# Kernel tuning notes

Measured on AMD Instinct MI355X. Metric: run time of the kernel, lower is better.

The kernel has to match this reference:

```python
import jax, jax.numpy as jnp
import numpy as np

N = 50000      # nodes
E = 800000     # edges (avg degree 16)
D = 128        # in_dim == hidden_dim
CD = 3         # coord_dim (SE(3))
L = 3          # num_layers


def setup_inputs() -> dict:
    key = jax.random.key(0)
    ks = jax.random.split(key, 10)
    s = np.float32(1.0 / np.sqrt(D))
    return {
        "x": jax.random.normal(ks[0], (N, D), jnp.float32),
        "pos": jax.random.normal(ks[1], (N, CD), jnp.float32),
        "edge_index": jax.random.randint(ks[2], (2, E), 0, N, dtype=jnp.int32),
        # per-layer stacked params (in_dim == hidden_dim so all layers stack)
        "Wl": jax.random.normal(ks[3], (L, D, D), jnp.float32) * s,
        "bl": jnp.zeros((L, D), jnp.float32),
        "Wc": jax.random.normal(ks[4], (L, D, 1), jnp.float32) * s,
        "bc": jnp.zeros((L, 1), jnp.float32),
        "WR": jax.random.normal(ks[5], (L, D, CD * CD), jnp.float32) * s,
        "bR": jnp.zeros((L, CD * CD), jnp.float32),
        "Wt": jax.random.normal(ks[6], (L, D, CD), jnp.float32) * s,
        "bt": jnp.zeros((L, CD), jnp.float32),
        # final fc
        "Wf": jax.random.normal(ks[7], (D, D), jnp.float32) * s,
        "bf": jnp.zeros((D,), jnp.float32),
    }


def reference(x, pos, edge_index, Wl, bl, Wc, bc, WR, bR, Wt, bt, Wf, bf):
    src, dst = edge_index[0], edge_index[1]
    n = x.shape[0]
    # R defaults to identity, t to zeros (R_dict/t_dict None path)
    R = jnp.broadcast_to(jnp.eye(CD, dtype=x.dtype), (n, CD, CD))
    t = jnp.zeros_like(pos)
    for i in range(L):
        h = x @ Wl[i] + bl[i]                          # (N, D)  per-edge-type linear
        # MessagePassing aggr='add': message x_j = h[src], scatter-add at dst
        out = jax.ops.segment_sum(h[src], dst, num_segments=n)  # (N, D)
        pos = pos + (out @ Wc[i] + bc[i])              # (N,3) + (N,1) broadcast
        R_upd = (out @ WR[i] + bR[i]).reshape(n, CD, CD)
        Q = jnp.linalg.qr(R_upd)[0]                    # orthonormalize rotation update
        R = Q @ R
        t = t + (out @ Wt[i] + bt[i])
        x = out
    z = x @ Wf + bf
    return z, pos, R, t
```

## Files before the change

### kernel.cpp

```cpp
#include <hip/hip_runtime.h>
#include <hip/hip_fp16.h>

typedef _Float16 half8 __attribute__((ext_vector_type(8)));
typedef float floatx4 __attribute__((ext_vector_type(4)));

#define NHC 16
#define WCOLS (128 + NHC)
#define OSH 13

__device__ inline void qr3_q(const double A[3][3], double Q[3][3]){
  double a[3][3];
#pragma unroll
  for (int r = 0; r < 3; r++)
#pragma unroll
    for (int c = 0; c < 3; c++) a[r][c] = A[r][c];

  double v1[3] = {1.0, 0.0, 0.0};
  double tau1 = 0.0;
  {
    double xn2 = a[1][0]*a[1][0] + a[2][0]*a[2][0];
    if (xn2 != 0.0){
      double alpha = a[0][0];
      double beta = -copysign(sqrt(alpha*alpha + xn2), alpha);
      tau1 = (beta - alpha) / beta;
      double inv = 1.0 / (alpha - beta);
      v1[1] = a[1][0] * inv;
      v1[2] = a[2][0] * inv;
#pragma unroll
      for (int c = 1; c < 3; c++){
        double w = a[0][c] + v1[1]*a[1][c] + v1[2]*a[2][c];
        double tw = tau1 * w;
        a[0][c] -= tw;
        a[1][c] -= tw * v1[1];
        a[2][c] -= tw * v1[2];
      }
    }
  }
  double tau2 = 0.0, v2 = 0.0;
  {
    double x2 = a[2][1];
    if (x2 != 0.0){
      double alpha = a[1][1];
      double beta = -copysign(sqrt(alpha*alpha + x2*x2), alpha);
      tau2 = (beta - alpha) / beta;
      v2 = x2 / (alpha - beta);
    }
  }
  double M[3][3] = {{1.0, 0.0, 0.0},
                    {0.0, 1.0 - tau2, -tau2*v2},
                    {0.0, -tau2*v2, 1.0 - tau2*v2*v2}};
#pragma unroll
  for (int c = 0; c < 3; c++){
    double w = v1[0]*M[0][c] + v1[1]*M[1][c] + v1[2]*M[2][c];
#pragma unroll
    for (int r = 0; r < 3; r++)
      Q[r][c] = M[r][c] - tau1 * v1[r] * w;
  }
}

__device__ inline void se3_node_ds(int n, const float ds[13],
                                   const float* __restrict__ bc, const float* __restrict__ bR,
                                   const float* __restrict__ bt, const float* __restrict__ pos_in,
                                   float* __restrict__ pos_o, float* __restrict__ R_o,
                                   float* __restrict__ t_o, int layer){
  double A[3][3], Q[3][3];
#pragma unroll
  for (int r = 0; r < 3; r++)
#pragma unroll
    for (int c = 0; c < 3; c++)
      A[r][c] = (double)ds[1 + r*3 + c] + (double)bR[r*3 + c];
  qr3_q(A, Q);

  double pd = (double)ds[0] + (double)bc[0];
#pragma unroll
  for (int c = 0; c < 3; c++){
    double base = (layer == 0) ? (double)pos_in[n*3 + c] : (double)pos_o[n*3 + c];
    pos_o[n*3 + c] = (float)(base + pd);
  }

  if (layer == 0){
#pragma unroll
    for (int r = 0; r < 3; r++)
#pragma unroll
      for (int c = 0; c < 3; c++)
        R_o[n*9 + r*3 + c] = (float)Q[r][c];
  } else {
    double Rold[3][3];
#pragma unroll
    for (int r = 0; r < 3; r++)
#pragma unroll
      for (int c = 0; c < 3; c++)
        Rold[r][c] = (double)R_o[n*9 + r*3 + c];
#pragma unroll
    for (int r = 0; r < 3; r++)
#pragma unroll
      for (int c = 0; c < 3; c++){
        double s = Q[r][0]*Rold[0][c] + Q[r][1]*Rold[1][c] + Q[r][2]*Rold[2][c];
        R_o[n*9 + r*3 + c] = (float)s;
      }
  }
#pragma unroll
  for (int c = 0; c < 3; c++){
    double base = (layer == 0) ? 0.0 : (double)t_o[n*3 + c];
    t_o[n*3 + c] = (float)(base + (double)ds[10 + c] + (double)bt[c]);
  }
}

__global__ void k_prep_w(const float* __restrict__ Wl, const float* __restrict__ Wf,
                         const float* __restrict__ Wc, const float* __restrict__ WR,
                         const float* __restrict__ Wt, _Float16* __restrict__ wTx,
                         int* __restrict__ cursor, int nbuck){
  int t = blockIdx.x*256 + threadIdx.x;
  if (blockIdx.x == 0 && threadIdx.x < nbuck) cursor[threadIdx.x] = 0;
  if (t >= 4*WCOLS*128) return;
  int l = t / (WCOLS*128);
  int rem = t - l*(WCOLS*128);
  int n = rem >> 7;
  int k = rem & 127;
  float v = 0.f;
  if (n < 128){
    const float* W = (l < 3) ? (Wl + (size_t)l*16384) : Wf;
    v = W[k*128 + n];
  } else if (l > 0){
    int h = n - 128, hl = l - 1;
    if (h == 0)       v = Wc[(size_t)hl*128 + k];
    else if (h < 10)  v = WR[(size_t)hl*128*9 + k*9 + (h-1)];
    else if (h < 13)  v = Wt[(size_t)hl*128*3 + k*3 + (h-10)];
  }
  wTx[t] = (_Float16)v;
}

__launch_bounds__(256)
__global__ void k_bin(const int* __restrict__ src, const int* __restrict__ dst,
                      int E, int nbuck, int capB,
                      int* __restrict__ cursor, int* __restrict__ binned){
  __shared__ int cnt[128];
  __shared__ int segbase[128];
  const int tid = threadIdx.x;
  for (int t = tid; t < nbuck; t += 256) cnt[t] = 0;
  __syncthreads();
  const int e0 = blockIdx.x*4096 + tid;
  int pk[16], bk[16];
#pragma unroll
  for (int j = 0; j < 16; j++){
    int e = e0 + j*256;
    if (e < E){
      int d = dst[e], s = src[e];
      bk[j] = d >> 9;
      pk[j] = (s << 9) | (d & 511);
      atomicAdd(&cnt[bk[j]], 1);
    } else bk[j] = -1;
  }
  __syncthreads();
  for (int t = tid; t < nbuck; t += 256){
    int c = cnt[t];
    if (c > 0) segbase[t] = t*capB + atomicAdd(&cursor[t], c);
    cnt[t] = 0;
  }
  __syncthreads();
#pragma unroll
  for (int j = 0; j < 16; j++){
    if (bk[j] >= 0){
      int ord = atomicAdd(&cnt[bk[j]], 1);
      binned[segbase[bk[j]] + ord] = pk[j];
    }
  }
}

__launch_bounds__(256)
__global__ void k_build(const int* __restrict__ binned, const int* __restrict__ cursor,
                        int N, int capB, int capC,
                        int2* __restrict__ sd, int* __restrict__ csr){
  __shared__ int deg2[512*8];
  __shared__ int lst2[512*8];
  __shared__ int cnt2[512*8];
  __shared__ int scn[256];
  const int b = blockIdx.x, tid = threadIdx.x;
  for (int t = tid; t < 512*8; t += 256){ deg2[t] = 0; cnt2[t] = 0; }
  __syncthreads();
  const int nE = cursor[b];
  const int gbase = b*capB;
  for (int i = tid; i < nE; i += 256){
    int v = binned[gbase + i];
    int o = v >> (9 + OSH);
    if (o > 7) o = 7;
    atomicAdd(&deg2[((v & 511) << 3) + o], 1);
  }
  __syncthreads();
  int d0 = 0, d1 = 0;
#pragma unroll
  for (int o = 0; o < 8; o++){ d0 += deg2[((2*tid) << 3) + o]; d1 += deg2[((2*tid+1) << 3) + o]; }
  const int p0 = (d0+7)&~7, p1 = (d1+7)&~7;
  scn[tid] = p0 + p1;
  __syncthreads();
#pragma unroll
  for (int off = 1; off < 256; off <<= 1){
    int add = (tid >= off) ? scn[tid-off] : 0;
    __syncthreads();
    scn[tid] += add;
    __syncthreads();
  }
  const int ex = scn[tid] - (p0 + p1);
  const int csrb = b*capC;
  {
    int off0 = ex;
#pragma unroll
    for (int o = 0; o < 8; o++){ lst2[((2*tid) << 3) + o] = off0; off0 += deg2[((2*tid) << 3) + o]; }
    int off1 = ex + p0;
#pragma unroll
    for (int o = 0; o < 8; o++){ lst2[((2*tid+1) << 3) + o] = off1; off1 += deg2[((2*tid+1) << 3) + o]; }
  }
  const int n0 = b*512 + 2*tid, n1 = n0 + 1;
  if (n0 < N) sd[n0] = make_int2(csrb + ex, p0);
  if (n1 < N) sd[n1] = make_int2(csrb + ex + p0, p1);
  __syncthreads();
  for (int i = tid; i < nE; i += 256){
    int v = binned[gbase + i];
    int dl = v & 511, s = v >> 9;
    int o = s >> OSH; if (o > 7) o = 7;
    int ord = atomicAdd(&cnt2[(dl << 3) + o], 1);
    csr[csrb + lst2[(dl << 3) + o] + ord] = s;
  }
  for (int j = d0; j < p0; j++) csr[csrb + ex + j] = N;
  for (int j = d1; j < p1; j++) csr[csrb + ex + p0 + j] = N;
}

__launch_bounds__(256)
__global__ void k_gemm_mfma(const void* __restrict__ Xin, const _Float16* __restrict__ Wt,
                            const float* __restrict__ bias, void* __restrict__ Hout,
                            int M, int in_fp32, int out_fp32, int zero_pad,
                            int se3_layer,
                            const float* __restrict__ bc, const float* __restrict__ bR,
                            const float* __restrict__ bt, const float* __restrict__ pos_in,
                            float* __restrict__ pos_o, float* __restrict__ R_o,
                            float* __restrict__ t_o, int N){
  __shared__ __align__(16) unsigned char lds[64*128*4 + 64*16*4];
  _Float16* lh = (_Float16*)lds;
  float*    lf = (float*)lds;
  float*    lheads = (float*)(lds + 64*128*4);

  const int tid  = threadIdx.x;
  const int wave = tid >> 6;
  const int lane = tid & 63;
  const int quad = lane >> 4;
  const int l16  = lane & 15;
  const int rbase0 = blockIdx.x*64;
  const int rbase  = rbase0 + (wave & 1)*32;
  const int cthi = wave >> 1;
  const int ctb = cthi*4;

  const _Float16* X16 = (const _Float16*)Xin;
  const float*    X32 = (const float*)Xin;

  half8 af[4][2];
#pragma unroll
  for (int kc = 0; kc < 4; kc++){
#pragma unroll
    for (int rt = 0; rt < 2; rt++){
      int r = rbase + rt*16 + l16;
      r = (r < M) ? r : (M - 1);
      if (in_fp32){
        const float* p = X32 + (size_t)r*128 + kc*32 + quad*8;
        float4 f0 = *(const float4*)p;
        float4 f1 = *(const float4*)(p + 4);
        half8 a;
        a[0]=(_Float16)f0.x; a[1]=(_Float16)f0.y; a[2]=(_Float16)f0.z; a[3]=(_Float16)f0.w;
        a[4]=(_Float16)f1.x; a[5]=(_Float16)f1.y; a[6]=(_Float16)f1.z; a[7]=(_Float16)f1.w;
        af[kc][rt] = a;
      } else {
        af[kc][rt] = *(const half8*)(X16 + (size_t)r*128 + kc*32 + quad*8);
      }
    }
  }

  floatx4 acc[2][5] = {};
#pragma unroll
  for (int kc = 0; kc < 4; kc++){
#pragma unroll
    for (int ct = 0; ct < 5; ct++){
      if (ct == 4 && cthi == 0) continue;
      half8 bf = *(const half8*)(Wt + (size_t)((ctb+ct)*16 + l16)*128 + kc*32 + quad*8);
      acc[0][ct] = __builtin_amdgcn_mfma_f32_16x16x32_f16(af[kc][0], bf, acc[0][ct], 0, 0, 0);
      acc[1][ct] = __builtin_amdgcn_mfma_f32_16x16x32_f16(af[kc][1], bf, acc[1][ct], 0, 0, 0);
    }
  }

#pragma unroll
  for (int rt = 0; rt < 2; rt++){
#pragma unroll
    for (int ct = 0; ct < 5; ct++){
      if (ct == 4 && cthi == 0) continue;
      int col = (ctb+ct)*16 + l16;
#pragma unroll
      for (int reg = 0; reg < 4; reg++){
        int rl = (wave & 1)*32 + rt*16 + quad*4 + reg;
        float v = acc[rt][ct][reg];
        if (col < 128){
          v += bias[col];
          if (out_fp32) lf[rl*128 + col] = v;
          else          lh[rl*128 + col] = (_Float16)v;
        } else {
          lheads[rl*16 + (col - 128)] = v;
        }
      }
    }
  }
  __syncthreads();

  if (out_fp32){
#pragma unroll
    for (int i = 0; i < 8; i++){
      int idx4 = i*256 + tid;
      int row = idx4 >> 5, c4 = idx4 & 31;
      int gr = rbase0 + row;
      if (gr < M)
        *(float4*)((float*)Hout + (size_t)gr*128 + c4*4) = *(const float4*)&lf[row*128 + c4*4];
    }
  } else {
#pragma unroll
    for (int i = 0; i < 4; i++){
      int idx8 = i*256 + tid;
      int row = idx8 >> 4, c8 = idx8 & 15;
      int gr = rbase0 + row;
      if (gr < M){
        *(half8*)((_Float16*)Hout + (size_t)gr*128 + c8*8) = *(const half8*)&lh[row*128 + c8*8];
      } else if (zero_pad && gr == M){
        half8 z = {};
        *(half8*)((_Float16*)Hout + (size_t)gr*128 + c8*8) = z;
      }
    }
  }

  if (se3_layer >= 0 && tid < 64){
    int n = rbase0 + tid;
    if (n < N){
      float ds[13];
#pragma unroll
      for (int c = 0; c < 13; c++) ds[c] = lheads[tid*16 + c];
      se3_node_ds(n, ds, bc, bR, bt, pos_in, pos_o, R_o, t_o, se3_layer);
    }
  }
}

__launch_bounds__(256)
__global__ void k_agg(const _Float16* __restrict__ H, const int* __restrict__ csr,
                      const int2* __restrict__ sd, _Float16* __restrict__ Xout, int N){
  const int wave = threadIdx.x >> 6;
  const int lane = threadIdx.x & 63;
  const int node = blockIdx.x*4 + wave;
  if (node >= N) return;
  int2 s = sd[node];
  const int s0 = s.x, degp = s.y;
  const unsigned int* Hu = (const unsigned int*)H;
  float acc0 = 0.f, acc1 = 0.f;
  for (int base = 0; base < degp; base += 64){
    int myidx = csr[s0 + base + lane];
    int m = degp - base; m = (m < 64) ? m : 64;
    for (int k = 0; k < m; k += 8){
      unsigned int v[8];
#pragma unroll
      for (int j = 0; j < 8; j++){
        int idx = __builtin_amdgcn_readlane(myidx, k + j);
        v[j] = Hu[(size_t)idx*64 + lane];
      }
#pragma unroll
      for (int j = 0; j < 8; j++){
        float2 f = __half22float2(*(__half2*)&v[j]);
        acc0 += f.x; acc1 += f.y;
      }
    }
  }
  __half2 ho = __floats2half2_rn(acc0, acc1);
  ((unsigned int*)Xout)[(size_t)node*64 + lane] = *(unsigned int*)&ho;
}

extern "C" void kernel_launch(void* const* d_in, const int* in_sizes, int n_in,
                              void* d_out, int out_size, void* d_ws, size_t ws_size,
                              hipStream_t stream){
  const float* x0  = (const float*)d_in[0];
  const float* pos = (const float*)d_in[1];
  const int*   ei  = (const int*)d_in[2];
  const float* Wl  = (const float*)d_in[3];
  const float* bl  = (const float*)d_in[4];
  const float* Wc  = (const float*)d_in[5];
  const float* bc  = (const float*)d_in[6];
  const float* WR  = (const float*)d_in[7];
  const float* bR  = (const float*)d_in[8];
  const float* Wt  = (const float*)d_in[9];
  const float* bt  = (const float*)d_in[10];
  const float* Wf  = (const float*)d_in[11];
  const float* bf  = (const float*)d_in[12];

  const int N = in_sizes[0] / 128;
  const int E = in_sizes[2] / 2;
  const int* srcp = ei;
  const int* dstp = ei + E;

  float* z_out = (float*)d_out;
  float* pos_o = z_out + (size_t)N*128;
  float* R_o   = pos_o + (size_t)N*3;
  float* t_o   = R_o   + (size_t)N*9;

  const int nbuck = (N + 511) >> 9;
  const int capB  = (((E + nbuck - 1)/nbuck)*5/4 + 256 + 63) & ~63;
  const int capC  = capB + 512*7;

  char* ws = (char*)d_ws;
  size_t off = 0;
  auto alloc = [&](size_t bytes)->char*{
    char* p = ws + off; off += (bytes + 511) & ~(size_t)511; return p;
  };
  _Float16* buf0h = (_Float16*)alloc((size_t)N*128*2);
  _Float16* buf1h = (_Float16*)alloc((size_t)(N+1)*128*2);
  _Float16* wTx   = (_Float16*)alloc((size_t)4*WCOLS*128*2);
  int2*  sd     = (int2*) alloc((size_t)N*8);
  int*   cursor = (int*)  alloc((size_t)nbuck*4);
  int*   binned = (int*)  alloc((size_t)nbuck*capB*4);
  int*   csr    = (int*)  alloc((size_t)nbuck*capC*4);

  k_prep_w<<<dim3((4*WCOLS*128 + 255)/256), dim3(256), 0, stream>>>(
      Wl, Wf, Wc, WR, Wt, wTx, cursor, nbuck);
  k_bin   <<<dim3((E + 4095)/4096), dim3(256), 0, stream>>>(srcp, dstp, E, nbuck, capB, cursor, binned);
  k_build <<<dim3(nbuck), dim3(256), 0, stream>>>(binned, cursor, N, capB, capC, sd, csr);

  const int gemm_blocks_pad = (N + 64)/64;
  const int gemm_blocks     = (N + 63)/64;
  const int agg_blocks      = (N + 3)/4;

  const void* xcur = (const void*)x0;
  for (int layer = 0; layer < 3; layer++){
    k_gemm_mfma<<<dim3(gemm_blocks_pad), dim3(256), 0, stream>>>(
        xcur, wTx + (size_t)layer*WCOLS*128, bl + (size_t)layer*128, (void*)buf1h,
        N, (layer == 0) ? 1 : 0, 0, 1,
        layer - 1, bc + (layer-1), bR + (size_t)(layer-1)*9, bt + (size_t)(layer-1)*3,
        pos, pos_o, R_o, t_o, N);
    k_agg<<<dim3(agg_blocks), dim3(256), 0, stream>>>(buf1h, csr, sd, buf0h, N);
    xcur = (const void*)buf0h;
  }
  k_gemm_mfma<<<dim3(gemm_blocks), dim3(256), 0, stream>>>(
      xcur, wTx + (size_t)3*WCOLS*128, bf, (void*)z_out,
      N, 0, 1, 0,
      2, bc + 2, bR + 18, bt + 6,
      pos, pos_o, R_o, t_o, N);
}
```

Measured before the change: 304.7 us.

## Aggregate before linear transform and fuse gather, GEMM and SE3 heads per layer

Reorders each layer as (A·X)·W + deg·b instead of A·(X·W + b), and stores the true in-degree alongside the padded degree for the bias term. Gather, GEMM and the SE3 head projection then run in a single kernel per layer, with the aggregated tile held in LDS. This removes a separate aggregation kernel and the H round trip through global memory. The heads are now computed from the freshly aggregated output inside the same layer. In exchange each block runs a serial per-wave gather over 16 nodes before its MFMA, and the input is converted to fp16 once up front.

```diff
diff --git a/kernel.cpp b/kernel.cpp
--- a/kernel.cpp
+++ b/kernel.cpp
@@ -4,8 +4,6 @@
 typedef _Float16 half8 __attribute__((ext_vector_type(8)));
 typedef float floatx4 __attribute__((ext_vector_type(4)));
 
-#define NHC 16
-#define WCOLS (128 + NHC)
 #define OSH 13
 
 __device__ inline void qr3_q(const double A[3][3], double Q[3][3]){
@@ -109,25 +107,44 @@
 __global__ void k_prep_w(const float* __restrict__ Wl, const float* __restrict__ Wf,
                          const float* __restrict__ Wc, const float* __restrict__ WR,
                          const float* __restrict__ Wt, _Float16* __restrict__ wTx,
+                         _Float16* __restrict__ wHd,
                          int* __restrict__ cursor, int nbuck){
   int t = blockIdx.x*256 + threadIdx.x;
   if (blockIdx.x == 0 && threadIdx.x < nbuck) cursor[threadIdx.x] = 0;
-  if (t >= 4*WCOLS*128) return;
-  int l = t / (WCOLS*128);
-  int rem = t - l*(WCOLS*128);
-  int n = rem >> 7;
-  int k = rem & 127;
-  float v = 0.f;
-  if (n < 128){
+  if (t < 4*128*128){
+    int l = t >> 14;
+    int n = (t >> 7) & 127;
+    int k = t & 127;
     const float* W = (l < 3) ? (Wl + (size_t)l*16384) : Wf;
-    v = W[k*128 + n];
-  } else if (l > 0){
-    int h = n - 128, hl = l - 1;
-    if (h == 0)       v = Wc[(size_t)hl*128 + k];
-    else if (h < 10)  v = WR[(size_t)hl*128*9 + k*9 + (h-1)];
-    else if (h < 13)  v = Wt[(size_t)hl*128*3 + k*3 + (h-10)];
-  }
-  wTx[t] = (_Float16)v;
+    wTx[t] = (_Float16)W[k*128 + n];
+  } else if (t < 4*128*128 + 3*16*128){
+    int u = t - 4*128*128;
+    int l = u >> 11;
+    int r = u & 2047;
+    int n = r >> 7;
+    int k = r & 127;
+    float v = 0.f;
+    if (n == 0)      v = Wc[(size_t)l*128 + k];
+    else if (n < 10) v = WR[(size_t)l*1152 + k*9 + (n-1)];
+    else if (n < 13) v = Wt[(size_t)l*384 + k*3 + (n-10)];
+    wHd[u] = (_Float16)v;
+  }
+}
+
+__launch_bounds__(256)
+__global__ void k_cvt(const float* __restrict__ x, _Float16* __restrict__ o, int N){
+  int c = blockIdx.x*256 + threadIdx.x;
+  if (c >= (N+1)*16) return;
+  int n = c >> 4;
+  half8 h = {};
+  if (n < N){
+    const float* p = x + (size_t)c*8;
+    float4 f0 = *(const float4*)p;
+    float4 f1 = *(const float4*)(p + 4);
+    h[0]=(_Float16)f0.x; h[1]=(_Float16)f0.y; h[2]=(_Float16)f0.z; h[3]=(_Float16)f0.w;
+    h[4]=(_Float16)f1.x; h[5]=(_Float16)f1.y; h[6]=(_Float16)f1.z; h[7]=(_Float16)f1.w;
+  }
+  *(half8*)(o + (size_t)c*8) = h;
 }
 
 __launch_bounds__(256)
@@ -211,8 +228,8 @@
     for (int o = 0; o < 8; o++){ lst2[((2*tid+1) << 3) + o] = off1; off1 += deg2[((2*tid+1) << 3) + o]; }
   }
   const int n0 = b*512 + 2*tid, n1 = n0 + 1;
-  if (n0 < N) sd[n0] = make_int2(csrb + ex, p0);
-  if (n1 < N) sd[n1] = make_int2(csrb + ex + p0, p1);
+  if (n0 < N) sd[n0] = make_int2(csrb + ex, (d0 << 16) | p0);
+  if (n1 < N) sd[n1] = make_int2(csrb + ex + p0, (d1 << 16) | p1);
   __syncthreads();
   for (int i = tid; i < nE; i += 256){
     int v = binned[gbase + i];
@@ -226,19 +243,144 @@
 }
 
 __launch_bounds__(256)
-__global__ void k_gemm_mfma(const void* __restrict__ Xin, const _Float16* __restrict__ Wt,
-                            const float* __restrict__ bias, void* __restrict__ Hout,
-                            int M, int in_fp32, int out_fp32, int zero_pad,
-                            int se3_layer,
-                            const float* __restrict__ bc, const float* __restrict__ bR,
-                            const float* __restrict__ bt, const float* __restrict__ pos_in,
-                            float* __restrict__ pos_o, float* __restrict__ R_o,
-                            float* __restrict__ t_o, int N){
-  __shared__ __align__(16) unsigned char lds[64*128*4 + 64*16*4];
-  _Float16* lh = (_Float16*)lds;
-  float*    lf = (float*)lds;
-  float*    lheads = (float*)(lds + 64*128*4);
-
+__global__ void k_fused(const _Float16* __restrict__ Xin,
+                        const _Float16* __restrict__ Wmain,
+                        const _Float16* __restrict__ Whd,
+                        const float* __restrict__ bias,
+                        const int* __restrict__ csr, const int2* __restrict__ sd,
+                        _Float16* __restrict__ Out,
+                        int N, int layer,
+                        const float* __restrict__ bc, const float* __restrict__ bR,
+                        const float* __restrict__ bt, const float* __restrict__ pos_in,
+                        float* __restrict__ pos_o, float* __restrict__ R_o,
+                        float* __restrict__ t_o){
+  __shared__ __align__(16) _Float16 lg[64][136];
+  __shared__ __align__(16) float lheads[64*16];
+  __shared__ float ldeg[64];
+
+  const int tid  = threadIdx.x;
+  const int wave = tid >> 6;
+  const int lane = tid & 63;
+  const int quad = lane >> 4;
+  const int l16  = lane & 15;
+  const int rbase0 = blockIdx.x*64;
+
+  {
+    const int nbase = rbase0 + wave*16;
+    int nn = nbase + (lane & 15);
+    int2 sv = (nn < N) ? sd[nn] : make_int2(0, 0);
+    const unsigned int* Xu = (const unsigned int*)Xin;
+    for (int i = 0; i < 16; i++){
+      int s0    = __builtin_amdgcn_readlane(sv.x, i);
+      int dpack = __builtin_amdgcn_readlane(sv.y, i);
+      int degp  = dpack & 0xffff;
+      if (lane == 0) ldeg[wave*16 + i] = (float)(dpack >> 16);
+      float acc0 = 0.f, acc1 = 0.f;
+      for (int base = 0; base < degp; base += 64){
+        int myidx = csr[s0 + base + lane];
+        int m = degp - base; m = (m < 64) ? m : 64;
+        for (int k = 0; k < m; k += 8){
+          unsigned int v[8];
+#pragma unroll
+          for (int j = 0; j < 8; j++){
+            int idx = __builtin_amdgcn_readlane(myidx, k + j);
+            v[j] = Xu[(size_t)idx*64 + lane];
+          }
+#pragma unroll
+          for (int j = 0; j < 8; j++){
+            float2 f = __half22float2(*(__half2*)&v[j]);
+            acc0 += f.x; acc1 += f.y;
+          }
+        }
+      }
+      __half2 ho = __floats2half2_rn(acc0, acc1);
+      ((unsigned int*)&lg[wave*16 + i][0])[lane] = *(unsigned int*)&ho;
+    }
+  }
+  __syncthreads();
+
+  const int cthi = wave >> 1;
+  half8 af[4][2];
+#pragma unroll
+  for (int kc = 0; kc < 4; kc++)
+#pragma unroll
+    for (int rt = 0; rt < 2; rt++){
+      int rl = (wave & 1)*32 + rt*16 + l16;
+      af[kc][rt] = *(const half8*)&lg[rl][kc*32 + quad*8];
+    }
+  __syncthreads();
+
+  floatx4 acc[2][4] = {};
+#pragma unroll
+  for (int kc = 0; kc < 4; kc++)
+#pragma unroll
+    for (int ct = 0; ct < 4; ct++){
+      half8 bf = *(const half8*)(Wmain + (size_t)((cthi*4 + ct)*16 + l16)*128 + kc*32 + quad*8);
+      acc[0][ct] = __builtin_amdgcn_mfma_f32_16x16x32_f16(af[kc][0], bf, acc[0][ct], 0, 0, 0);
+      acc[1][ct] = __builtin_amdgcn_mfma_f32_16x16x32_f16(af[kc][1], bf, acc[1][ct], 0, 0, 0);
+    }
+
+#pragma unroll
+  for (int rt = 0; rt < 2; rt++){
+    float dgv[4];
+#pragma unroll
+    for (int reg = 0; reg < 4; reg++)
+      dgv[reg] = ldeg[(wave & 1)*32 + rt*16 + quad*4 + reg];
+#pragma unroll
+    for (int ct = 0; ct < 4; ct++){
+      int col = (cthi*4 + ct)*16 + l16;
+      float b = bias[col];
+#pragma unroll
+      for (int reg = 0; reg < 4; reg++){
+        int rl = (wave & 1)*32 + rt*16 + quad*4 + reg;
+        lg[rl][col] = (_Float16)(acc[rt][ct][reg] + b*dgv[reg]);
+      }
+    }
+  }
+  __syncthreads();
+
+#pragma unroll
+  for (int i = 0; i < 4; i++){
+    int idx8 = i*256 + tid;
+    int row = idx8 >> 4, c8 = idx8 & 15;
+    int gr = rbase0 + row;
+    if (gr < N){
+      *(half8*)(Out + (size_t)gr*128 + c8*8) = *(const half8*)&lg[row][c8*8];
+    } else if (gr == N){
+      half8 z = {};
+      *(half8*)(Out + (size_t)gr*128 + c8*8) = z;
+    }
+  }
+
+  {
+    floatx4 hacc = {};
+#pragma unroll
+    for (int kc = 0; kc < 4; kc++){
+      half8 ha = *(const half8*)&lg[wave*16 + l16][kc*32 + quad*8];
+      half8 bf = *(const half8*)(Whd + (size_t)l16*128 + kc*32 + quad*8);
+      hacc = __builtin_amdgcn_mfma_f32_16x16x32_f16(ha, bf, hacc, 0, 0, 0);
+    }
+#pragma unroll
+    for (int reg = 0; reg < 4; reg++)
+      lheads[(wave*16 + quad*4 + reg)*16 + l16] = hacc[reg];
+  }
+  __syncthreads();
+
+  if (tid < 64){
+    int n = rbase0 + tid;
+    if (n < N){
+      float ds[13];
+#pragma unroll
+      for (int c = 0; c < 13; c++) ds[c] = lheads[tid*16 + c];
+      se3_node_ds(n, ds, bc, bR, bt, pos_in, pos_o, R_o, t_o, layer);
+    }
+  }
+}
+
+__launch_bounds__(256)
+__global__ void k_final(const _Float16* __restrict__ X, const _Float16* __restrict__ Wmain,
+                        const float* __restrict__ bias, float* __restrict__ Z, int M){
+  __shared__ __align__(16) float lf[64][128];
   const int tid  = threadIdx.x;
   const int wave = tid >> 6;
   const int lane = tid & 63;
@@ -247,131 +389,49 @@
   const int rbase0 = blockIdx.x*64;
   const int rbase  = rbase0 + (wave & 1)*32;
   const int cthi = wave >> 1;
-  const int ctb = cthi*4;
-
-  const _Float16* X16 = (const _Float16*)Xin;
-  const float*    X32 = (const float*)Xin;
 
   half8 af[4][2];
 #pragma unroll
-  for (int kc = 0; kc < 4; kc++){
+  for (int kc = 0; kc < 4; kc++)
 #pragma unroll
     for (int rt = 0; rt < 2; rt++){
       int r = rbase + rt*16 + l16;
       r = (r < M) ? r : (M - 1);
-      if (in_fp32){
-        const float* p = X32 + (size_t)r*128 + kc*32 + quad*8;
-        float4 f0 = *(const float4*)p;
-        float4 f1 = *(const float4*)(p + 4);
-        half8 a;
-        a[0]=(_Float16)f0.x; a[1]=(_Float16)f0.y; a[2]=(_Float16)f0.z; a[3]=(_Float16)f0.w;
-        a[4]=(_Float16)f1.x; a[5]=(_Float16)f1.y; a[6]=(_Float16)f1.z; a[7]=(_Float16)f1.w;
-        af[kc][rt] = a;
-      } else {
-        af[kc][rt] = *(const half8*)(X16 + (size_t)r*128 + kc*32 + quad*8);
-      }
-    }
-  }
-
-  floatx4 acc[2][5] = {};
-#pragma unroll
-  for (int kc = 0; kc < 4; kc++){
-#pragma unroll
-    for (int ct = 0; ct < 5; ct++){
-      if (ct == 4 && cthi == 0) continue;
-      half8 bf = *(const half8*)(Wt + (size_t)((ctb+ct)*16 + l16)*128 + kc*32 + quad*8);
+      af[kc][rt] = *(const half8*)(X + (size_t)r*128 + kc*32 + quad*8);
+    }
+
+  floatx4 acc[2][4] = {};
+#pragma unroll
+  for (int kc = 0; kc < 4; kc++)
+#pragma unroll
+    for (int ct = 0; ct < 4; ct++){
+      half8 bf = *(const half8*)(Wmain + (size_t)((cthi*4 + ct)*16 + l16)*128 + kc*32 + quad*8);
       acc[0][ct] = __builtin_amdgcn_mfma_f32_16x16x32_f16(af[kc][0], bf, acc[0][ct], 0, 0, 0);
       acc[1][ct] = __builtin_amdgcn_mfma_f32_16x16x32_f16(af[kc][1], bf, acc[1][ct], 0, 0, 0);
     }
-  }
-
-#pragma unroll
-  for (int rt = 0; rt < 2; rt++){
-#pragma unroll
-    for (int ct = 0; ct < 5; ct++){
-      if (ct == 4 && cthi == 0) continue;
-      int col = (ctb+ct)*16 + l16;
+
+#pragma unroll
+  for (int rt = 0; rt < 2; rt++)
+#pragma unroll
+    for (int ct = 0; ct < 4; ct++){
+      int col = (cthi*4 + ct)*16 + l16;
+      float b = bias[col];
 #pragma unroll
       for (int reg = 0; reg < 4; reg++){
         int rl = (wave & 1)*32 + rt*16 + quad*4 + reg;
-        float v = acc[rt][ct][reg];
-        if (col < 128){
-          v += bias[col];
-          if (out_fp32) lf[rl*128 + col] = v;
-          else          lh[rl*128 + col] = (_Float16)v;
-        } else {
-          lheads[rl*16 + (col - 128)] = v;
-        }
+        lf[rl][col] = acc[rt][ct][reg] + b;
       }
     }
-  }
-  __syncthreads();
-
-  if (out_fp32){
-#pragma unroll
-    for (int i = 0; i < 8; i++){
-      int idx4 = i*256 + tid;
-      int row = idx4 >> 5, c4 = idx4 & 31;
-      int gr = rbase0 + row;
-      if (gr < M)
-        *(float4*)((float*)Hout + (size_t)gr*128 + c4*4) = *(const float4*)&lf[row*128 + c4*4];
-    }
-  } else {
-#pragma unroll
-    for (int i = 0; i < 4; i++){
-      int idx8 = i*256 + tid;
-      int row = idx8 >> 4, c8 = idx8 & 15;
-      int gr = rbase0 + row;
-      if (gr < M){
-        *(half8*)((_Float16*)Hout + (size_t)gr*128 + c8*8) = *(const half8*)&lh[row*128 + c8*8];
-      } else if (zero_pad && gr == M){
-        half8 z = {};
-        *(half8*)((_Float16*)Hout + (size_t)gr*128 + c8*8) = z;
-      }
-    }
-  }
-
-  if (se3_layer >= 0 && tid < 64){
-    int n = rbase0 + tid;
-    if (n < N){
-      float ds[13];
-#pragma unroll
-      for (int c = 0; c < 13; c++) ds[c] = lheads[tid*16 + c];
-      se3_node_ds(n, ds, bc, bR, bt, pos_in, pos_o, R_o, t_o, se3_layer);
-    }
-  }
-}
-
-__launch_bounds__(256)
-__global__ void k_agg(const _Float16* __restrict__ H, const int* __restrict__ csr,
-                      const int2* __restrict__ sd, _Float16* __restrict__ Xout, int N){
-  const int wave = threadIdx.x >> 6;
-  const int lane = threadIdx.x & 63;
-  const int node = blockIdx.x*4 + wave;
-  if (node >= N) return;
-  int2 s = sd[node];
-  const int s0 = s.x, degp = s.y;
-  const unsigned int* Hu = (const unsigned int*)H;
-  float acc0 = 0.f, acc1 = 0.f;
-  for (int base = 0; base < degp; base += 64){
-    int myidx = csr[s0 + base + lane];
-    int m = degp - base; m = (m < 64) ? m : 64;
-    for (int k = 0; k < m; k += 8){
-      unsigned int v[8];
-#pragma unroll
-      for (int j = 0; j < 8; j++){
-        int idx = __builtin_amdgcn_readlane(myidx, k + j);
-        v[j] = Hu[(size_t)idx*64 + lane];
-      }
-#pragma unroll
-      for (int j = 0; j < 8; j++){
-        float2 f = __half22float2(*(__half2*)&v[j]);
-        acc0 += f.x; acc1 += f.y;
-      }
-    }
-  }
-  __half2 ho = __floats2half2_rn(acc0, acc1);
-  ((unsigned int*)Xout)[(size_t)node*64 + lane] = *(unsigned int*)&ho;
+  __syncthreads();
+
+#pragma unroll
+  for (int i = 0; i < 8; i++){
+    int idx4 = i*256 + tid;
+    int row = idx4 >> 5, c4 = idx4 & 31;
+    int gr = rbase0 + row;
+    if (gr < M)
+      *(float4*)(Z + (size_t)gr*128 + c4*4) = *(const float4*)&lf[row][c4*4];
+  }
 }
 
 extern "C" void kernel_launch(void* const* d_in, const int* in_sizes, int n_in,
@@ -410,36 +470,35 @@
   auto alloc = [&](size_t bytes)->char*{
     char* p = ws + off; off += (bytes + 511) & ~(size_t)511; return p;
   };
-  _Float16* buf0h = (_Float16*)alloc((size_t)N*128*2);
-  _Float16* buf1h = (_Float16*)alloc((size_t)(N+1)*128*2);
-  _Float16* wTx   = (_Float16*)alloc((size_t)4*WCOLS*128*2);
+  _Float16* bufA = (_Float16*)alloc((size_t)(N+1)*128*2);
+  _Float16* bufB = (_Float16*)alloc((size_t)(N+1)*128*2);
+  _Float16* wTx  = (_Float16*)alloc((size_t)4*128*128*2);
+  _Float16* wHd  = (_Float16*)alloc((size_t)3*16*128*2);
   int2*  sd     = (int2*) alloc((size_t)N*8);
   int*   cursor = (int*)  alloc((size_t)nbuck*4);
   int*   binned = (int*)  alloc((size_t)nbuck*capB*4);
   int*   csr    = (int*)  alloc((size_t)nbuck*capC*4);
 
-  k_prep_w<<<dim3((4*WCOLS*128 + 255)/256), dim3(256), 0, stream>>>(
-      Wl, Wf, Wc, WR, Wt, wTx, cursor, nbuck);
+  const int prep_total = 4*128*128 + 3*16*128;
+  k_prep_w<<<dim3((prep_total + 255)/256), dim3(256), 0, stream>>>(
+      Wl, Wf, Wc, WR, Wt, wTx, wHd, cursor, nbuck);
   k_bin   <<<dim3((E + 4095)/4096), dim3(256), 0, stream>>>(srcp, dstp, E, nbuck, capB, cursor, binned);
   k_build <<<dim3(nbuck), dim3(256), 0, stream>>>(binned, cursor, N, capB, capC, sd, csr);
-
-  const int gemm_blocks_pad = (N + 64)/64;
-  const int gemm_blocks     = (N + 63)/64;
-  const int agg_blocks      = (N + 3)/4;
-
-  const void* xcur = (const void*)x0;
+  k_cvt   <<<dim3(((N+1)*16 + 255)/256), dim3(256), 0, stream>>>(x0, bufA, N);
+
+  const int fused_blocks = (N + 64) >> 6;
+  const int final_blocks = (N + 63) >> 6;
+
+  const _Float16* xin = bufA;
+  _Float16* xout = bufB;
   for (int layer = 0; layer < 3; layer++){
-    k_gemm_mfma<<<dim3(gemm_blocks_pad), dim3(256), 0, stream>>>(
-        xcur, wTx + (size_t)layer*WCOLS*128, bl + (size_t)layer*128, (void*)buf1h,
-        N, (layer == 0) ? 1 : 0, 0, 1,
-        layer - 1, bc + (layer-1), bR + (size_t)(layer-1)*9, bt + (size_t)(layer-1)*3,
-        pos, pos_o, R_o, t_o, N);
-    k_agg<<<dim3(agg_blocks), dim3(256), 0, stream>>>(buf1h, csr, sd, buf0h, N);
-    xcur = (const void*)buf0h;
-  }
-  k_gemm_mfma<<<dim3(gemm_blocks), dim3(256), 0, stream>>>(
-      xcur, wTx + (size_t)3*WCOLS*128, bf, (void*)z_out,
-      N, 0, 1, 0,
-      2, bc + 2, bR + 18, bt + 6,
-      pos, pos_o, R_o, t_o, N);
-}
+    k_fused<<<dim3(fused_blocks), dim3(256), 0, stream>>>(
+        xin, wTx + (size_t)layer*16384, wHd + (size_t)layer*2048, bl + (size_t)layer*128,
+        csr, sd, xout, N, layer,
+        bc + layer, bR + (size_t)layer*9, bt + (size_t)layer*3,
+        pos, pos_o, R_o, t_o);
+    const _Float16* tmp = xin; xin = xout; xout = (_Float16*)tmp;
+  }
+  k_final<<<dim3(final_blocks), dim3(256), 0, stream>>>(
+      xin, wTx + (size_t)3*16384, bf, z_out, N);
+}
```

New measurement: 283.0 us. 1.08x faster.
